# Kernel tuning notes

Hardware: AMD Instinct MI355X
Metric: run time of the kernel (lower is better)

The kernel has to match this reference:

```python
import jax, jax.numpy as jnp
import numpy as np

B, T, D, H = 16, 512, 512, 8
TE = 2048
DH = D // H


def _ln(x, g, b, eps=1e-5):
    m = jnp.mean(x, axis=-1, keepdims=True)
    v = jnp.mean((x - m) ** 2, axis=-1, keepdims=True)
    return (x - m) * jax.lax.rsqrt(v + eps) * g + b


def setup_inputs() -> dict:
    key = jax.random.key(0)
    ks = jax.random.split(key, 16)
    s = 0.02
    inp = {
        "x1": jax.random.normal(ks[0], (B, T, D), jnp.float32),
        "x2": jax.random.normal(ks[1], (B, T, D), jnp.float32),
        "emb": jax.random.normal(ks[2], (2 * B, TE), jnp.float32),
        "src_mask": jnp.ones((2 * B, T, T, 1), jnp.float32),
        # LayerNorm params (x-norm and text-norm)
        "ln_x_g": jnp.ones((D,), jnp.float32), "ln_x_b": jnp.zeros((D,), jnp.float32),
        "ln_t_g": jnp.ones((D,), jnp.float32), "ln_t_b": jnp.zeros((D,), jnp.float32),
        # Q/K/V projections, stored as [in, out]
        "Wq": jax.random.normal(ks[3], (D, D), jnp.float32) * s, "bq": jnp.zeros((D,), jnp.float32),
        "Wk": jax.random.normal(ks[4], (D, D), jnp.float32) * s, "bk": jnp.zeros((D,), jnp.float32),
        "Wv": jax.random.normal(ks[5], (D, D), jnp.float32) * s, "bv": jnp.zeros((D,), jnp.float32),
        # StylizationBlock: SiLU->Linear(TE, 2D), LayerNorm(D), SiLU->Linear(D, D)
        "Wemb": jax.random.normal(ks[6], (TE, 2 * D), jnp.float32) * s, "bemb": jnp.zeros((2 * D,), jnp.float32),
        "sb_g": jnp.ones((D,), jnp.float32), "sb_b": jnp.zeros((D,), jnp.float32),
        "Wout": jax.random.normal(ks[7], (D, D), jnp.float32) * s, "bout": jnp.zeros((D,), jnp.float32),
    }
    return inp


def reference(x1, x2, emb, src_mask,
              ln_x_g, ln_x_b, ln_t_g, ln_t_b,
              Wq, bq, Wk, bk, Wv, bv,
              Wemb, bemb, sb_g, sb_b, Wout, bout):
    # cross=True: swap-concat the two interacting streams
    xa = jnp.concatenate([x1, x2], axis=0)  # [2B,T,D] (query side)
    xb = jnp.concatenate([x2, x1], axis=0)  # [2B,T,D] (key/value side)
    B2 = xa.shape[0]

    xn = _ln(xa, ln_x_g, ln_x_b)
    tn = _ln(xb, ln_t_g, ln_t_b)

    q = (xn @ Wq + bq).reshape(B2, T, H, DH)
    k = (tn @ Wk + bk).reshape(B2, T, H, DH)
    v = (tn @ Wv + bv).reshape(B2, T, H, DH)

    attn = jnp.einsum('bnhd,bmhd->bnmh', q, k) / np.sqrt(DH).astype(np.float32)
    attn = attn + (1.0 - src_mask) * -100000.0
    w = jax.nn.softmax(attn, axis=2)  # softmax over key axis m

    y = jnp.einsum('bnmh,bmhd->bnhd', w, v).reshape(B2, T, D)

    # StylizationBlock: FiLM from emb, then SiLU + Linear
    emb_out = (jax.nn.silu(emb) @ Wemb + bemb)[:, None, :]  # [2B,1,2D]
    scale, shift = jnp.split(emb_out, 2, axis=2)
    h = _ln(y, sb_g, sb_b) * (1.0 + scale) + shift
    h = jax.nn.silu(h) @ Wout + bout

    out = xa + h
    return out[:B2 // 2], out[B2 // 2:]
```

## Files before the change

### kernel.cpp

```cpp
#include <hip/hip_runtime.h>
#include <hip/hip_bf16.h>
#include <stdint.h>


typedef float f32x4 __attribute__((ext_vector_type(4)));
typedef short s16x8 __attribute__((ext_vector_type(8)));

#define MFMA16(a, b, c) __builtin_amdgcn_mfma_f32_16x16x32_bf16((a), (b), (c), 0, 0, 0)
#define GLD16(g, l) __builtin_amdgcn_global_load_lds( \
    (const __attribute__((address_space(1))) void*)(g), \
    (__attribute__((address_space(3))) void*)(l), 16, 0, 0)

__device__ __forceinline__ ushort f2bf(float f) {
    union { float f; uint32_t u; } cv; cv.f = f;
    uint32_t u = cv.u;
    return (ushort)((u + 0x7fffu + ((u >> 16) & 1u)) >> 16);
}
__device__ __forceinline__ float bf2f(ushort u) {
    union { uint32_t u; float f; } cv; cv.u = ((uint32_t)u) << 16;
    return cv.f;
}
__device__ __forceinline__ uint32_t pack_bf2(float a, float b) {
    union { float f; uint32_t u; } x, y; x.f = a; y.f = b;
    return ((x.u + 0x8000u) >> 16) | ((y.u + 0x8000u) & 0xffff0000u);
}
__device__ __forceinline__ float fast_exp2(float x) {
#if __has_builtin(__builtin_amdgcn_exp2f)
    return __builtin_amdgcn_exp2f(x);
#else
    return exp2f(x);
#endif
}
__device__ __forceinline__ float wave_sum(float v) {
#pragma unroll
    for (int o = 32; o > 0; o >>= 1) v += __shfl_xor(v, o);
    return v;
}

#define QSCALE 0.180336880f
#define MNEG  -144269.504f

__global__ __launch_bounds__(256) void wconv(
    const float* __restrict__ w0, const float* __restrict__ w1,
    const float* __restrict__ w2, const float* __restrict__ w3,
    ushort* __restrict__ o0, ushort* __restrict__ o1,
    ushort* __restrict__ o2, ushort* __restrict__ o3) {
    const float* src; ushort* dst;
    switch (blockIdx.z) {
        case 0: src = w0; dst = o0; break;
        case 1: src = w1; dst = o1; break;
        case 2: src = w2; dst = o2; break;
        default: src = w3; dst = o3; break;
    }
    __shared__ float tile[32][33];
    const int n0 = blockIdx.x * 32, k0 = blockIdx.y * 32;
    const int x = threadIdx.x & 31, y0 = threadIdx.x >> 5;
#pragma unroll
    for (int i = 0; i < 4; i++) {
        int yy = y0 + 8 * i;
        tile[yy][x] = src[(size_t)(k0 + yy) * 512 + n0 + x];
    }
    __syncthreads();
#pragma unroll
    for (int i = 0; i < 4; i++) {
        int yy = y0 + 8 * i;
        dst[(size_t)(n0 + yy) * 512 + k0 + x] = f2bf(tile[x][yy]);
    }
}

__global__ __launch_bounds__(256) void ln_prep(
    const float* __restrict__ x1, const float* __restrict__ x2,
    const float* __restrict__ gx, const float* __restrict__ bx,
    const float* __restrict__ gt, const float* __restrict__ bt,
    ushort* __restrict__ xn, ushort* __restrict__ tn) {
    const int r = blockIdx.x * 4 + (threadIdx.x >> 6);
    const int lane = threadIdx.x & 63;
    const float* src = (r < 8192) ? x1 + (size_t)r * 512
                                  : x2 + (size_t)(r - 8192) * 512;
    const int tr = (r < 8192) ? r + 8192 : r - 8192;
    const int d0 = lane * 4;

    float4 a0 = *(const float4*)&src[d0];
    float4 a1 = *(const float4*)&src[d0 + 256];
    float s = a0.x + a0.y + a0.z + a0.w + a1.x + a1.y + a1.z + a1.w;
    float q = a0.x*a0.x + a0.y*a0.y + a0.z*a0.z + a0.w*a0.w
            + a1.x*a1.x + a1.y*a1.y + a1.z*a1.z + a1.w*a1.w;
    s = wave_sum(s); q = wave_sum(q);
    const float mean = s * (1.f/512.f);
    const float var = q * (1.f/512.f) - mean * mean;
    const float rs = rsqrtf(var + 1e-5f);

    float vals[8] = {a0.x, a0.y, a0.z, a0.w, a1.x, a1.y, a1.z, a1.w};
    ushort* px = xn + (size_t)r * 512;
    ushort* pt = tn + (size_t)tr * 512;
#pragma unroll
    for (int half = 0; half < 2; half++) {
        ushort4 ox, ot;
        ushort* pox = (ushort*)&ox; ushort* pot = (ushort*)&ot;
#pragma unroll
        for (int j = 0; j < 4; j++) {
            int d = d0 + half * 256 + j;
            float nv = (vals[half * 4 + j] - mean) * rs;
            pox[j] = f2bf(nv * gx[d] + bx[d]);
            pot[j] = f2bf(nv * gt[d] + bt[d]);
        }
        *(ushort4*)&px[d0 + half * 256] = ox;
        *(ushort4*)&pt[d0 + half * 256] = ot;
    }
}

__global__ __launch_bounds__(1024) void maskchk(const float* __restrict__ mask,
                                                int* __restrict__ flags) {
    __shared__ int f8[8];
    const int b2 = blockIdx.x, qt = blockIdx.y, tid = threadIdx.x;
    if (tid < 8) f8[tid] = 0;
    __syncthreads();
    int bad8 = 0;
#pragma unroll
    for (int jj = 0; jj < 8; jj++) {
        int fi = jj * 1024 + tid;
        int row = fi >> 7, col4 = fi & 127, ktl = col4 >> 4;
        float4 v = *(const float4*)&mask[((size_t)(b2 * 512 + qt * 64 + row)) * 512 + col4 * 4];
        if (v.x != 1.f || v.y != 1.f || v.z != 1.f || v.w != 1.f) bad8 |= 1 << ktl;
    }
    if (bad8) {
#pragma unroll
        for (int kt = 0; kt < 8; kt++)
            if ((bad8 >> kt) & 1) atomicOr(&f8[kt], 1);
    }
    __syncthreads();
    if (tid < 8) flags[(b2 * 8 + qt) * 8 + tid] = f8[tid];
}

__global__ __launch_bounds__(256) void emb_init(const float* __restrict__ bemb,
                                                float* __restrict__ ss) {
    int i = blockIdx.x * 256 + threadIdx.x;
    ss[i] = bemb[i & 1023];
}

__global__ __launch_bounds__(256) void emb_gemm(const float* __restrict__ emb,
                                                const float* __restrict__ Wemb,
                                                float* __restrict__ ss) {
    __shared__ float es[32 * 128];
    const int n0 = blockIdx.x * 128, k0 = blockIdx.y * 128;
    const int t = threadIdx.x;
#pragma unroll
    for (int i = 0; i < 16; i++) {
        int idx = t + 256 * i;
        int b = idx >> 7, kk = idx & 127;
        float v = emb[(size_t)b * 2048 + k0 + kk];
        es[idx] = v / (1.f + __expf(-v));
    }
    __syncthreads();
    const int n = n0 + (t & 127);
    const int kh = (t >> 7) * 64;
    float acc[32];
#pragma unroll
    for (int b = 0; b < 32; b++) acc[b] = 0.f;
    for (int kk = kh; kk < kh + 64; kk++) {
        float w = Wemb[(size_t)(k0 + kk) * 1024 + n];
#pragma unroll
        for (int b = 0; b < 32; b++) acc[b] += es[b * 128 + kk] * w;
    }
#pragma unroll
    for (int b = 0; b < 32; b++) atomicAdd(&ss[b * 1024 + n], acc[b]);
}

__global__ __launch_bounds__(256) void gemm_qkv(
    const ushort* __restrict__ xn, const ushort* __restrict__ tn,
    const ushort* __restrict__ W,
    const float* __restrict__ bq, const float* __restrict__ bk,
    const float* __restrict__ bv,
    ushort* __restrict__ qb, ushort* __restrict__ kb,
    ushort* __restrict__ vtb) {
    __shared__ ushort As[128 * 64];
    __shared__ ushort Bs[128 * 64];
    const int tid = threadIdx.x;
    const int lane = tid & 63, w = tid >> 6;
    const int l15 = lane & 15, quad = lane >> 4;
    const int l8 = lane >> 3, c_src = (lane & 7) ^ l8;
    const int bid = blockIdx.x;
    const int xcd = bid & 7, j = bid >> 3;
    const int mt_l = j / 12, nt = j % 12;
    const int m0 = (xcd * 16 + mt_l) * 128, n0 = nt * 128;
    const ushort* A = (n0 < 512) ? xn : tn;
    const int wm = (w >> 1) * 64, wn = (w & 1) * 64;

    f32x4 zero = {0.f, 0.f, 0.f, 0.f};
    f32x4 acc[4][4];
#pragma unroll
    for (int i = 0; i < 4; i++)
#pragma unroll
        for (int jj = 0; jj < 4; jj++) acc[i][jj] = zero;

    const ushort* ga0 = A + (size_t)(m0 + w * 32 + l8) * 512 + c_src * 8;
    const ushort* gb0 = W + (size_t)(n0 + w * 32 + l8) * 512 + c_src * 8;

    for (int k0 = 0; k0 < 512; k0 += 64) {
#pragma unroll
        for (int i = 0; i < 4; i++) {
            GLD16(ga0 + (size_t)(i * 8) * 512 + k0, &As[(w * 32 + i * 8) * 64]);
            GLD16(gb0 + (size_t)(i * 8) * 512 + k0, &Bs[(w * 32 + i * 8) * 64]);
        }
        __syncthreads();
#pragma unroll
        for (int ks = 0; ks < 2; ks++) {
            const int sl = ((ks * 4 + quad) ^ (l15 & 7)) * 8;
            s16x8 af[4], bf[4];
#pragma unroll
            for (int i = 0; i < 4; i++)
                af[i] = *(const s16x8*)&As[(wm + i * 16 + l15) * 64 + sl];
#pragma unroll
            for (int jj = 0; jj < 4; jj++)
                bf[jj] = *(const s16x8*)&Bs[(wn + jj * 16 + l15) * 64 + sl];
#pragma unroll
            for (int i = 0; i < 4; i++)
#pragma unroll
                for (int jj = 0; jj < 4; jj++)
                    acc[i][jj] = MFMA16(af[i], bf[jj], acc[i][jj]);
        }
        __syncthreads();
    }

#pragma unroll
    for (int i = 0; i < 4; i++)
#pragma unroll
        for (int jj = 0; jj < 4; jj++) {
            const int col = n0 + wn + jj * 16 + l15;
            if (n0 < 512) {
                const float bvv = bq[col];
#pragma unroll
                for (int reg = 0; reg < 4; reg++) {
                    const int row = m0 + wm + i * 16 + quad * 4 + reg;
                    qb[(size_t)row * 512 + col] = f2bf((acc[i][jj][reg] + bvv) * QSCALE);
                }
            } else if (n0 < 1024) {
                const int ck = col - 512;
                const float bvv = bk[ck];
#pragma unroll
                for (int reg = 0; reg < 4; reg++) {
                    const int row = m0 + wm + i * 16 + quad * 4 + reg;
                    kb[(size_t)row * 512 + ck] = f2bf(acc[i][jj][reg] + bvv);
                }
            } else {
                const int c2 = col - 1024;
                const float bvv = bv[c2];
                const int b2 = m0 >> 9;
                const int t0 = (m0 & 511) + wm + i * 16 + quad * 4;
                ushort4 o4; ushort* po = (ushort*)&o4;
#pragma unroll
                for (int reg = 0; reg < 4; reg++)
                    po[reg] = f2bf(acc[i][jj][reg] + bvv);
                *(ushort4*)&vtb[((size_t)((b2 * 8 + (c2 >> 6)) * 64 + (c2 & 63))) * 512 + t0] = o4;
            }
        }
}

__global__ __launch_bounds__(256) void gemm_out(
    const ushort* __restrict__ A, const ushort* __restrict__ Bt,
    const float* __restrict__ bias, float* __restrict__ of,
    const float* __restrict__ r1, const float* __restrict__ r2) {
    __shared__ ushort As[128 * 64];
    __shared__ ushort Bs[128 * 64];
    const int tid = threadIdx.x;
    const int lane = tid & 63, w = tid >> 6;
    const int l15 = lane & 15, quad = lane >> 4;
    const int l8 = lane >> 3, c_src = (lane & 7) ^ l8;
    const int bid = blockIdx.x;
    const int xcd = bid & 7, j2 = bid >> 3;
    const int m0 = (xcd * 16 + (j2 >> 2)) * 128;
    const int n0 = (j2 & 3) * 128;
    const int wm = (w >> 1) * 64, wn = (w & 1) * 64;

    f32x4 zero = {0.f, 0.f, 0.f, 0.f};
    f32x4 acc[4][4];
#pragma unroll
    for (int i = 0; i < 4; i++)
#pragma unroll
        for (int jj = 0; jj < 4; jj++) acc[i][jj] = zero;

    const ushort* ga0 = A + (size_t)(m0 + w * 32 + l8) * 512 + c_src * 8;
    const ushort* gb0 = Bt + (size_t)(n0 + w * 32 + l8) * 512 + c_src * 8;

    for (int k0 = 0; k0 < 512; k0 += 64) {
#pragma unroll
        for (int i = 0; i < 4; i++) {
            GLD16(ga0 + (size_t)(i * 8) * 512 + k0, &As[(w * 32 + i * 8) * 64]);
            GLD16(gb0 + (size_t)(i * 8) * 512 + k0, &Bs[(w * 32 + i * 8) * 64]);
        }
        __syncthreads();
#pragma unroll
        for (int ks = 0; ks < 2; ks++) {
            const int sl = ((ks * 4 + quad) ^ (l15 & 7)) * 8;
            s16x8 af[4], bf[4];
#pragma unroll
            for (int i = 0; i < 4; i++)
                af[i] = *(const s16x8*)&As[(wm + i * 16 + l15) * 64 + sl];
#pragma unroll
            for (int jj = 0; jj < 4; jj++)
                bf[jj] = *(const s16x8*)&Bs[(wn + jj * 16 + l15) * 64 + sl];
#pragma unroll
            for (int i = 0; i < 4; i++)
#pragma unroll
                for (int jj = 0; jj < 4; jj++)
                    acc[i][jj] = MFMA16(af[i], bf[jj], acc[i][jj]);
        }
        __syncthreads();
    }

#pragma unroll
    for (int i = 0; i < 4; i++)
#pragma unroll
        for (int jj = 0; jj < 4; jj++) {
            const int col = n0 + wn + jj * 16 + l15;
            const float bvv = bias[col];
#pragma unroll
            for (int reg = 0; reg < 4; reg++) {
                const int row = m0 + wm + i * 16 + quad * 4 + reg;
                float res = (row < 8192)
                                ? r1[(size_t)row * 512 + col]
                                : r2[(size_t)(row - 8192) * 512 + col];
                of[(size_t)row * 512 + col] = acc[i][jj][reg] + bvv + res;
            }
        }
}

__global__ __launch_bounds__(256) void attn(
    const ushort* __restrict__ q, const ushort* __restrict__ k,
    const ushort* __restrict__ vt, const float* __restrict__ mask,
    const int* __restrict__ flags, ushort* __restrict__ y) {
    __shared__ ushort Ks[2][64 * 64];
    __shared__ ushort Vs[2][64 * 64];
    __shared__ ushort Ps[4][16 * 72];
    const int tid = threadIdx.x;
    const int lane = tid & 63, w = tid >> 6;
    const int l15 = lane & 15, quad = lane >> 4;
    const int l8 = lane >> 3, c_src = (lane & 7) ^ l8;
    const int bh = blockIdx.x, qt = blockIdx.y;
    const int b2 = bh >> 3, h = bh & 7;
    const int qrow0 = qt * 64 + w * 16;

    s16x8 qf0, qf1;
    {
        const ushort* qp = q + ((size_t)(b2 * 512 + qrow0 + l15)) * 512 + h * 64 + quad * 8;
        qf0 = *(const s16x8*)qp;
        qf1 = *(const s16x8*)(qp + 32);
    }
    f32x4 zero = {0.f, 0.f, 0.f, 0.f};
    f32x4 o[4];
#pragma unroll
    for (int nt = 0; nt < 4; nt++) o[nt] = zero;
    float l_i = 0.f;

    const ushort* kg0 = k + ((size_t)(b2 * 512 + w * 16 + l8)) * 512 + h * 64 + c_src * 8;
    const ushort* vg0 = vt + ((size_t)(bh * 64 + w * 16 + l8)) * 512 + c_src * 8;
    ushort* Pw = &Ps[w][0];
    const int slq = (quad ^ (l15 & 7)) * 8;
    const int slq4 = ((4 + quad) ^ (l15 & 7)) * 8;
    const int fl_base = (b2 * 8 + qt) * 8;

    auto stage = [&](int buf, int kt) {
        GLD16(kg0 + (size_t)(kt * 64) * 512, &Ks[buf][(w * 16) * 64]);
        GLD16(kg0 + (size_t)(kt * 64 + 8) * 512, &Ks[buf][(w * 16 + 8) * 64]);
        GLD16(vg0 + kt * 64, &Vs[buf][(w * 16) * 64]);
        GLD16(vg0 + (size_t)8 * 512 + kt * 64, &Vs[buf][(w * 16 + 8) * 64]);
    };
    stage(0, 0);

    for (int kt = 0; kt < 8; kt++) {
        __syncthreads();
        if (kt < 7) stage((kt + 1) & 1, kt + 1);
        const ushort* Kb = Ks[kt & 1];
        const ushort* Vb = Vs[kt & 1];

        f32x4 st[4];
#pragma unroll
        for (int mt = 0; mt < 4; mt++) {
            const int row = (mt * 16 + l15) * 64;
            s16x8 kf0 = *(const s16x8*)&Kb[row + slq];
            s16x8 kf1 = *(const s16x8*)&Kb[row + slq4];
            st[mt] = MFMA16(kf0, qf0, zero);
            st[mt] = MFMA16(kf1, qf1, st[mt]);
        }

        if (flags[fl_base + kt]) {
            const size_t mb = ((size_t)(b2 * 512 + qt * 64 + w * 16 + l15)) * 512 + kt * 64;
#pragma unroll
            for (int mt = 0; mt < 4; mt++)
#pragma unroll
                for (int reg = 0; reg < 4; reg++)
                    st[mt][reg] += (1.f - mask[mb + mt * 16 + quad * 4 + reg]) * MNEG;
        }

        float psum = 0.f;
#pragma unroll
        for (int mt = 0; mt < 4; mt++) {
            float p0 = fast_exp2(st[mt][0]);
            float p1 = fast_exp2(st[mt][1]);
            float p2 = fast_exp2(st[mt][2]);
            float p3 = fast_exp2(st[mt][3]);
            psum += (p0 + p1) + (p2 + p3);
            uint2 pk;
            pk.x = pack_bf2(p0, p1);
            pk.y = pack_bf2(p2, p3);
            *(uint2*)&Pw[l15 * 72 + mt * 16 + quad * 4] = pk;
        }

        s16x8 pf0 = *(const s16x8*)&Pw[l15 * 72 + quad * 8];
        s16x8 pf1 = *(const s16x8*)&Pw[l15 * 72 + 32 + quad * 8];
#pragma unroll
        for (int nt = 0; nt < 4; nt++) {
            const int vr = (nt * 16 + l15) * 64;
            s16x8 vf0 = *(const s16x8*)&Vb[vr + slq];
            s16x8 vf1 = *(const s16x8*)&Vb[vr + slq4];
            o[nt] = MFMA16(pf0, vf0, o[nt]);
            o[nt] = MFMA16(pf1, vf1, o[nt]);
        }

        psum += __shfl_xor(psum, 16);
        psum += __shfl_xor(psum, 32);
        l_i += psum;
    }

    const float invl = 1.f / l_i;
    float ir[4];
#pragma unroll
    for (int reg = 0; reg < 4; reg++) ir[reg] = __shfl(invl, quad * 4 + reg);
#pragma unroll
    for (int reg = 0; reg < 4; reg++) {
        const int row = qt * 64 + w * 16 + quad * 4 + reg;
        ushort* yp = y + ((size_t)(b2 * 512 + row)) * 512 + h * 64;
#pragma unroll
        for (int nt = 0; nt < 4; nt++)
            yp[nt * 16 + l15] = f2bf(o[nt][reg] * ir[reg]);
    }
}

__global__ __launch_bounds__(256) void film_silu(
    const ushort* __restrict__ y, const float* __restrict__ g,
    const float* __restrict__ b, const float* __restrict__ ss,
    ushort* __restrict__ tb) {
    const int r = blockIdx.x * 4 + (threadIdx.x >> 6);
    const int lane = threadIdx.x & 63;
    const int b2 = r >> 9;
    const int d0 = lane * 8;
    s16x8 raw = *(const s16x8*)&y[(size_t)r * 512 + d0];
    float v[8];
#pragma unroll
    for (int j = 0; j < 8; j++) v[j] = bf2f((ushort)raw[j]);
    float s = 0.f, qq = 0.f;
#pragma unroll
    for (int j = 0; j < 8; j++) { s += v[j]; qq += v[j] * v[j]; }
    s = wave_sum(s); qq = wave_sum(qq);
    const float mean = s * (1.f/512.f);
    const float var = qq * (1.f/512.f) - mean * mean;
    const float rs = rsqrtf(var + 1e-5f);
    const float* scp = ss + (size_t)b2 * 1024;
    s16x8 o;
#pragma unroll
    for (int j = 0; j < 8; j++) {
        int d = d0 + j;
        float ln = (v[j] - mean) * rs * g[d] + b[d];
        float hv = ln * (1.f + scp[d]) + scp[512 + d];
        o[j] = (short)f2bf(hv / (1.f + __expf(-hv)));
    }
    *(s16x8*)&tb[(size_t)r * 512 + d0] = o;
}

extern "C" void kernel_launch(void* const* d_in, const int* in_sizes, int n_in,
                              void* d_out, int out_size, void* d_ws, size_t ws_size,
                              hipStream_t stream) {
    const float* x1     = (const float*)d_in[0];
    const float* x2     = (const float*)d_in[1];
    const float* emb    = (const float*)d_in[2];
    const float* mask   = (const float*)d_in[3];
    const float* ln_x_g = (const float*)d_in[4];
    const float* ln_x_b = (const float*)d_in[5];
    const float* ln_t_g = (const float*)d_in[6];
    const float* ln_t_b = (const float*)d_in[7];
    const float* Wq     = (const float*)d_in[8];
    const float* bq     = (const float*)d_in[9];
    const float* Wk     = (const float*)d_in[10];
    const float* bk     = (const float*)d_in[11];
    const float* Wv     = (const float*)d_in[12];
    const float* bv     = (const float*)d_in[13];
    const float* Wemb   = (const float*)d_in[14];
    const float* bemb   = (const float*)d_in[15];
    const float* sb_g   = (const float*)d_in[16];
    const float* sb_b   = (const float*)d_in[17];
    const float* Wout   = (const float*)d_in[18];
    const float* bout   = (const float*)d_in[19];
    float* out = (float*)d_out;

    char* ws = (char*)d_ws;
    ushort* xn   = (ushort*)(ws + 0);
    ushort* tn   = (ushort*)(ws + (16u << 20));
    ushort* qb   = (ushort*)(ws + (32u << 20));
    ushort* kb   = (ushort*)(ws + (48u << 20));
    ushort* vtb  = (ushort*)(ws + (64u << 20));
    ushort* yb   = (ushort*)(ws + (80u << 20));
    ushort* wqkv = (ushort*)(ws + (96u << 20));
    ushort* wto  = wqkv + 786432;
    float*  ss   = (float*)(ws + (98u << 20));
    int*    flg  = (int*)(ws + (98u << 20) + (128u << 10));
    ushort* tb   = xn;

    wconv<<<dim3(16, 16, 4), 256, 0, stream>>>(Wq, Wk, Wv, Wout,
                                               wqkv, wqkv + 262144, wqkv + 524288, wto);
    ln_prep<<<4096, 256, 0, stream>>>(x1, x2, ln_x_g, ln_x_b, ln_t_g, ln_t_b, xn, tn);
    maskchk<<<dim3(32, 8), 1024, 0, stream>>>(mask, flg);
    emb_init<<<128, 256, 0, stream>>>(bemb, ss);
    emb_gemm<<<dim3(8, 16), 256, 0, stream>>>(emb, Wemb, ss);

    gemm_qkv<<<1536, 256, 0, stream>>>(xn, tn, wqkv, bq, bk, bv, qb, kb, vtb);

    attn<<<dim3(256, 8), 256, 0, stream>>>(qb, kb, vtb, mask, flg, yb);

    film_silu<<<4096, 256, 0, stream>>>(yb, sb_g, sb_b, ss, tb);

    gemm_out<<<512, 256, 0, stream>>>(tb, wto, bout, out, x1, x2);

    (void)in_sizes; (void)n_in; (void)out_size; (void)ws_size;
}
```

Before: 309.2 us.

## Merge preprocessing kernels into one launch and set GEMM occupancy bounds

Folds the weight conversion, LayerNorm prep, mask check and emb bias init into a single kernel that dispatches on block index, removing three kernel launches and letting the independent work overlap. The mask check is rebuilt as one 256-thread block per 64x64 tile that uses a wave ballot instead of shared-memory atomics. Both GEMM kernels also get a minimum-blocks-per-SM hint of 3, which may cap register use and cause spills.

```diff
diff --git a/kernel.cpp b/kernel.cpp
--- a/kernel.cpp
+++ b/kernel.cpp
@@ -40,102 +40,96 @@
 #define QSCALE 0.180336880f
 #define MNEG  -144269.504f
 
-__global__ __launch_bounds__(256) void wconv(
+__global__ __launch_bounds__(256) void prep(
     const float* __restrict__ w0, const float* __restrict__ w1,
     const float* __restrict__ w2, const float* __restrict__ w3,
     ushort* __restrict__ o0, ushort* __restrict__ o1,
-    ushort* __restrict__ o2, ushort* __restrict__ o3) {
-    const float* src; ushort* dst;
-    switch (blockIdx.z) {
-        case 0: src = w0; dst = o0; break;
-        case 1: src = w1; dst = o1; break;
-        case 2: src = w2; dst = o2; break;
-        default: src = w3; dst = o3; break;
-    }
-    __shared__ float tile[32][33];
-    const int n0 = blockIdx.x * 32, k0 = blockIdx.y * 32;
-    const int x = threadIdx.x & 31, y0 = threadIdx.x >> 5;
-#pragma unroll
-    for (int i = 0; i < 4; i++) {
-        int yy = y0 + 8 * i;
-        tile[yy][x] = src[(size_t)(k0 + yy) * 512 + n0 + x];
-    }
-    __syncthreads();
-#pragma unroll
-    for (int i = 0; i < 4; i++) {
-        int yy = y0 + 8 * i;
-        dst[(size_t)(n0 + yy) * 512 + k0 + x] = f2bf(tile[x][yy]);
-    }
-}
-
-__global__ __launch_bounds__(256) void ln_prep(
+    ushort* __restrict__ o2, ushort* __restrict__ o3,
     const float* __restrict__ x1, const float* __restrict__ x2,
     const float* __restrict__ gx, const float* __restrict__ bx,
     const float* __restrict__ gt, const float* __restrict__ bt,
-    ushort* __restrict__ xn, ushort* __restrict__ tn) {
-    const int r = blockIdx.x * 4 + (threadIdx.x >> 6);
-    const int lane = threadIdx.x & 63;
-    const float* src = (r < 8192) ? x1 + (size_t)r * 512
-                                  : x2 + (size_t)(r - 8192) * 512;
-    const int tr = (r < 8192) ? r + 8192 : r - 8192;
-    const int d0 = lane * 4;
-
-    float4 a0 = *(const float4*)&src[d0];
-    float4 a1 = *(const float4*)&src[d0 + 256];
-    float s = a0.x + a0.y + a0.z + a0.w + a1.x + a1.y + a1.z + a1.w;
-    float q = a0.x*a0.x + a0.y*a0.y + a0.z*a0.z + a0.w*a0.w
-            + a1.x*a1.x + a1.y*a1.y + a1.z*a1.z + a1.w*a1.w;
-    s = wave_sum(s); q = wave_sum(q);
-    const float mean = s * (1.f/512.f);
-    const float var = q * (1.f/512.f) - mean * mean;
-    const float rs = rsqrtf(var + 1e-5f);
-
-    float vals[8] = {a0.x, a0.y, a0.z, a0.w, a1.x, a1.y, a1.z, a1.w};
-    ushort* px = xn + (size_t)r * 512;
-    ushort* pt = tn + (size_t)tr * 512;
-#pragma unroll
-    for (int half = 0; half < 2; half++) {
-        ushort4 ox, ot;
-        ushort* pox = (ushort*)&ox; ushort* pot = (ushort*)&ot;
+    ushort* __restrict__ xn, ushort* __restrict__ tn,
+    const float* __restrict__ mask, int* __restrict__ flags,
+    const float* __restrict__ bemb, float* __restrict__ ss) {
+    __shared__ float tile[32][33];
+    __shared__ int bad4[4];
+    const int bid = blockIdx.x, tid = threadIdx.x;
+
+    if (bid < 1024) {
+        const int z = bid >> 8, xy = bid & 255;
+        const float* src; ushort* dst;
+        switch (z) {
+            case 0: src = w0; dst = o0; break;
+            case 1: src = w1; dst = o1; break;
+            case 2: src = w2; dst = o2; break;
+            default: src = w3; dst = o3; break;
+        }
+        const int n0 = (xy & 15) * 32, k0 = (xy >> 4) * 32;
+        const int x = tid & 31, y0 = tid >> 5;
+#pragma unroll
+        for (int i = 0; i < 4; i++) {
+            int yy = y0 + 8 * i;
+            tile[yy][x] = src[(size_t)(k0 + yy) * 512 + n0 + x];
+        }
+        __syncthreads();
+#pragma unroll
+        for (int i = 0; i < 4; i++) {
+            int yy = y0 + 8 * i;
+            dst[(size_t)(n0 + yy) * 512 + k0 + x] = f2bf(tile[x][yy]);
+        }
+    } else if (bid < 5120) {
+        const int r = (bid - 1024) * 4 + (tid >> 6);
+        const int lane = tid & 63;
+        const float* src = (r < 8192) ? x1 + (size_t)r * 512
+                                      : x2 + (size_t)(r - 8192) * 512;
+        const int tr = (r < 8192) ? r + 8192 : r - 8192;
+        const int d0 = lane * 4;
+        float4 a0 = *(const float4*)&src[d0];
+        float4 a1 = *(const float4*)&src[d0 + 256];
+        float s = a0.x + a0.y + a0.z + a0.w + a1.x + a1.y + a1.z + a1.w;
+        float q = a0.x*a0.x + a0.y*a0.y + a0.z*a0.z + a0.w*a0.w
+                + a1.x*a1.x + a1.y*a1.y + a1.z*a1.z + a1.w*a1.w;
+        s = wave_sum(s); q = wave_sum(q);
+        const float mean = s * (1.f/512.f);
+        const float var = q * (1.f/512.f) - mean * mean;
+        const float rs = rsqrtf(var + 1e-5f);
+        float vals[8] = {a0.x, a0.y, a0.z, a0.w, a1.x, a1.y, a1.z, a1.w};
+        ushort* px = xn + (size_t)r * 512;
+        ushort* pt = tn + (size_t)tr * 512;
+#pragma unroll
+        for (int half = 0; half < 2; half++) {
+            ushort4 ox, ot;
+            ushort* pox = (ushort*)&ox; ushort* pot = (ushort*)&ot;
+#pragma unroll
+            for (int j = 0; j < 4; j++) {
+                int d = d0 + half * 256 + j;
+                float nv = (vals[half * 4 + j] - mean) * rs;
+                pox[j] = f2bf(nv * gx[d] + bx[d]);
+                pot[j] = f2bf(nv * gt[d] + bt[d]);
+            }
+            *(ushort4*)&px[d0 + half * 256] = ox;
+            *(ushort4*)&pt[d0 + half * 256] = ot;
+        }
+    } else if (bid < 7168) {
+        const int b = bid - 5120;
+        const int b2 = b >> 6, qt = (b >> 3) & 7, kt = b & 7;
+        const int r = tid >> 2, c4 = tid & 3;
+        const float* mrow = mask + ((size_t)(b2 * 512 + qt * 64 + r)) * 512 + kt * 64;
+        bool bad = false;
 #pragma unroll
         for (int j = 0; j < 4; j++) {
-            int d = d0 + half * 256 + j;
-            float nv = (vals[half * 4 + j] - mean) * rs;
-            pox[j] = f2bf(nv * gx[d] + bx[d]);
-            pot[j] = f2bf(nv * gt[d] + bt[d]);
-        }
-        *(ushort4*)&px[d0 + half * 256] = ox;
-        *(ushort4*)&pt[d0 + half * 256] = ot;
-    }
-}
-
-__global__ __launch_bounds__(1024) void maskchk(const float* __restrict__ mask,
-                                                int* __restrict__ flags) {
-    __shared__ int f8[8];
-    const int b2 = blockIdx.x, qt = blockIdx.y, tid = threadIdx.x;
-    if (tid < 8) f8[tid] = 0;
-    __syncthreads();
-    int bad8 = 0;
-#pragma unroll
-    for (int jj = 0; jj < 8; jj++) {
-        int fi = jj * 1024 + tid;
-        int row = fi >> 7, col4 = fi & 127, ktl = col4 >> 4;
-        float4 v = *(const float4*)&mask[((size_t)(b2 * 512 + qt * 64 + row)) * 512 + col4 * 4];
-        if (v.x != 1.f || v.y != 1.f || v.z != 1.f || v.w != 1.f) bad8 |= 1 << ktl;
-    }
-    if (bad8) {
-#pragma unroll
-        for (int kt = 0; kt < 8; kt++)
-            if ((bad8 >> kt) & 1) atomicOr(&f8[kt], 1);
-    }
-    __syncthreads();
-    if (tid < 8) flags[(b2 * 8 + qt) * 8 + tid] = f8[tid];
-}
-
-__global__ __launch_bounds__(256) void emb_init(const float* __restrict__ bemb,
-                                                float* __restrict__ ss) {
-    int i = blockIdx.x * 256 + threadIdx.x;
-    ss[i] = bemb[i & 1023];
+            float4 v = *(const float4*)&mrow[(c4 + 4 * j) * 4];
+            bad |= (v.x != 1.f) | (v.y != 1.f) | (v.z != 1.f) | (v.w != 1.f);
+        }
+        unsigned long long bl = __ballot(bad);
+        const int w = tid >> 6;
+        if ((tid & 63) == 0) bad4[w] = (bl != 0ull);
+        __syncthreads();
+        if (tid == 0) flags[b] = bad4[0] | bad4[1] | bad4[2] | bad4[3];
+    } else {
+        int i = (bid - 7168) * 256 + tid;
+        ss[i] = bemb[i & 1023];
+    }
 }
 
 __global__ __launch_bounds__(256) void emb_gemm(const float* __restrict__ emb,
@@ -166,7 +160,7 @@
     for (int b = 0; b < 32; b++) atomicAdd(&ss[b * 1024 + n], acc[b]);
 }
 
-__global__ __launch_bounds__(256) void gemm_qkv(
+__global__ __launch_bounds__(256, 3) void gemm_qkv(
     const ushort* __restrict__ xn, const ushort* __restrict__ tn,
     const ushort* __restrict__ W,
     const float* __restrict__ bq, const float* __restrict__ bk,
@@ -256,7 +250,7 @@
         }
 }
 
-__global__ __launch_bounds__(256) void gemm_out(
+__global__ __launch_bounds__(256, 3) void gemm_out(
     const ushort* __restrict__ A, const ushort* __restrict__ Bt,
     const float* __restrict__ bias, float* __restrict__ of,
     const float* __restrict__ r1, const float* __restrict__ r2) {
@@ -505,11 +499,11 @@
     int*    flg  = (int*)(ws + (98u << 20) + (128u << 10));
     ushort* tb   = xn;
 
-    wconv<<<dim3(16, 16, 4), 256, 0, stream>>>(Wq, Wk, Wv, Wout,
-                                               wqkv, wqkv + 262144, wqkv + 524288, wto);
-    ln_prep<<<4096, 256, 0, stream>>>(x1, x2, ln_x_g, ln_x_b, ln_t_g, ln_t_b, xn, tn);
-    maskchk<<<dim3(32, 8), 1024, 0, stream>>>(mask, flg);
-    emb_init<<<128, 256, 0, stream>>>(bemb, ss);
+    prep<<<7296, 256, 0, stream>>>(Wq, Wk, Wv, Wout,
+                                   wqkv, wqkv + 262144, wqkv + 524288, wto,
+                                   x1, x2, ln_x_g, ln_x_b, ln_t_g, ln_t_b, xn, tn,
+                                   mask, flg, bemb, ss);
+
     emb_gemm<<<dim3(8, 16), 256, 0, stream>>>(emb, Wemb, ss);
 
     gemm_qkv<<<1536, 256, 0, stream>>>(xn, tn, wqkv, bq, bk, bv, qb, kb, vtb);
```

After: 294.3 us. -4.8%, faster.
